# Kernel tuning notes

Measured on AMD Instinct MI355X. Metric: run time of the kernel, lower is better.

## Reference

```python
import jax, jax.numpy as jnp
import numpy as np

B, P, ENC = 64, 196, 512
E, H, A, V, L = 1024, 1024, 512, 20000, 25


def setup_inputs() -> dict:
    key = jax.random.key(0)
    ks = jax.random.split(key, 20)
    s = 0.02
    return {
        "encoder_out": jax.random.normal(ks[0], (B, P, ENC), jnp.float32),
        "captions": jax.random.randint(ks[1], (B, L), 0, V),
        "lengths": L,
        # attention MLP
        "W_enc_att": jax.random.normal(ks[2], (ENC, A), jnp.float32) * s,
        "b_enc_att": jnp.zeros((A,), jnp.float32),
        "W_dec_att": jax.random.normal(ks[3], (H, A), jnp.float32) * s,
        "b_dec_att": jnp.zeros((A,), jnp.float32),
        "W_full_att": jax.random.normal(ks[4], (A, 1), jnp.float32) * s,
        "b_full_att": jnp.zeros((1,), jnp.float32),
        # embedding
        "emb_table": jax.random.normal(ks[5], (V, E), jnp.float32) * s,
        # LSTMCell: input = embedding + context -> (E+ENC, 4H)
        "W_ih": jax.random.normal(ks[6], (E + ENC, 4 * H), jnp.float32) * s,
        "b_ih": jnp.zeros((4 * H,), jnp.float32),
        "W_hh": jax.random.normal(ks[7], (H, 4 * H), jnp.float32) * s,
        "b_hh": jnp.zeros((4 * H,), jnp.float32),
        # init states
        "W_init_h": jax.random.normal(ks[8], (ENC, H), jnp.float32) * s,
        "b_init_h": jnp.zeros((H,), jnp.float32),
        "W_init_c": jax.random.normal(ks[9], (ENC, H), jnp.float32) * s,
        "b_init_c": jnp.zeros((H,), jnp.float32),
        # gate + output proj
        "W_fbeta": jax.random.normal(ks[10], (H, ENC), jnp.float32) * s,
        "b_fbeta": jnp.zeros((ENC,), jnp.float32),
        "W_fc": jax.random.normal(ks[11], (H, V), jnp.float32) * s,
        "b_fc": jnp.zeros((V,), jnp.float32),
    }


def _decode(encoder_out, W_enc_att, b_enc_att, W_dec_att, b_dec_att,
            W_full_att, b_full_att, emb_table, W_ih, b_ih, W_hh, b_hh,
            W_init_h, b_init_h, W_init_c, b_init_c, W_fbeta, b_fbeta,
            W_fc, b_fc, captions, T):
    # precompute encoder-side attention projection (constant across timesteps)
    att_enc = encoder_out @ W_enc_att + b_enc_att          # (B, P, A)
    mean_feat = encoder_out.mean(axis=1)                   # (B, ENC)
    h0 = mean_feat @ W_init_h + b_init_h
    c0 = mean_feat @ W_init_c + b_init_c
    embeddings = emb_table[captions[:, :T]]                # (B, T, E)
    xs = jnp.swapaxes(embeddings, 0, 1)                    # (T, B, E)

    def step(carry, emb_t):
        h, c = carry
        att_dec = h @ W_dec_att + b_dec_att                # (B, A)
        energy = (jax.nn.relu(att_enc + att_dec[:, None, :]) @ W_full_att
                  + b_full_att)[..., 0]                    # (B, P)
        alpha = jax.nn.softmax(energy, axis=1)
        context = jnp.einsum('bp,bpe->be', alpha, encoder_out)
        gate = jax.nn.sigmoid(h @ W_fbeta + b_fbeta)       # (B, ENC)
        x = jnp.concatenate([emb_t, gate * context], axis=1)
        gates = x @ W_ih + b_ih + h @ W_hh + b_hh          # (B, 4H)
        i, f, g, o = jnp.split(gates, 4, axis=1)           # torch order i,f,g,o
        c = jax.nn.sigmoid(f) * c + jax.nn.sigmoid(i) * jnp.tanh(g)
        h = jax.nn.sigmoid(o) * jnp.tanh(c)
        preds = h @ W_fc + b_fc                            # dropout = identity (eval)
        return (h, c), (preds, alpha)

    _, (preds, alphas) = jax.lax.scan(step, (h0, c0), xs)
    predictions = jnp.swapaxes(preds, 0, 1)                # (B, T, V)
    alphas = jnp.swapaxes(alphas, 0, 1)                    # (B, T, P)
    return predictions, alphas


def reference(encoder_out, captions, lengths, W_enc_att, b_enc_att, W_dec_att,
              b_dec_att, W_full_att, b_full_att, emb_table, W_ih, b_ih, W_hh,
              b_hh, W_init_h, b_init_h, W_init_c, b_init_c, W_fbeta, b_fbeta,
              W_fc, b_fc):
    T = int(lengths) - 1
    return _decode(encoder_out, W_enc_att, b_enc_att, W_dec_att, b_dec_att,
                   W_full_att, b_full_att, emb_table, W_ih, b_ih, W_hh, b_hh,
                   W_init_h, b_init_h, W_init_c, b_init_c, W_fbeta, b_fbeta,
                   W_fc, b_fc, captions, T)
```

## Files before the change

### kernel.cpp

```cpp
#include <hip/hip_runtime.h>
#include <hip/hip_bf16.h>

#define BB 64
#define PP 196
#define ENCD 512
#define ED 1024
#define HD 1024
#define AD 512
#define VD 20000
#define TT 24
#define VPAD 20096
#define NSA 4

typedef __attribute__((ext_vector_type(8))) short short8;
typedef __attribute__((ext_vector_type(4))) short short4v;
typedef __attribute__((ext_vector_type(4))) float f32x4;

__device__ __forceinline__ float sigf(float x) { return 1.f / (1.f + __expf(-x)); }

__device__ __forceinline__ unsigned short f2bf(float f) {
    unsigned u = __builtin_bit_cast(unsigned, f);
    u = (u + 0x7FFFu + ((u >> 16) & 1u)) >> 16;
    return (unsigned short)u;
}
__device__ __forceinline__ void split2(float v, unsigned short& h, unsigned short& l) {
    h = f2bf(v);
    float hf = __builtin_bit_cast(float, ((unsigned)h) << 16);
    l = f2bf(v - hf);
}

__global__ __launch_bounds__(256) void split_w_kernel(
    const float* __restrict__ W, unsigned short* __restrict__ oh,
    unsigned short* __restrict__ ol, int N , int Npad, int coff,
    int Nlaunch, int rowoff, int perm) {
    int n = blockIdx.x * 256 + threadIdx.x;
    if (n >= Nlaunch) return;
    int kc = blockIdx.y;
    int src = perm ? ((n & 3) * 1024 + (n >> 2)) : n;
    short8 vh, vl;
    #pragma unroll
    for (int j = 0; j < 8; ++j) {
        float v = (src < N) ? W[(size_t)(rowoff + kc * 8 + j) * N + src] : 0.f;
        unsigned short h, l; split2(v, h, l);
        vh[j] = (short)h; vl[j] = (short)l;
    }
    size_t o = ((size_t)kc * Npad + coff + n) * 8;
    *(short8*)(oh + o) = vh; *(short8*)(ol + o) = vl;
}

__global__ __launch_bounds__(256) void embed_f32_kernel(
    const int* __restrict__ captions, const float* __restrict__ table,
    float* __restrict__ emb_f) {
    int t = blockIdx.x, b = blockIdx.y;
    int tok = captions[b * 25 + t];
    const float4* src = (const float4*)(table + (size_t)tok * ED);
    float4* dst = (float4*)(emb_f + ((size_t)t * BB + b) * ED);
    dst[threadIdx.x] = src[threadIdx.x];
}

__global__ __launch_bounds__(256) void bias_perm_kernel(
    const float* __restrict__ b_ih, const float* __restrict__ b_hh,
    float* __restrict__ out) {
    int n = blockIdx.x * 256 + threadIdx.x;
    int src = (n & 3) * 1024 + (n >> 2);
    out[n] = b_ih[src] + b_hh[src];
}

__global__ __launch_bounds__(512) void mean_kernel(const float* __restrict__ enc,
                                                   float* __restrict__ mf) {
    int b = blockIdx.x; int e = threadIdx.x;
    const float* base = enc + (size_t)b * PP * ENCD + e;
    float s = 0.f;
    #pragma unroll 4
    for (int p = 0; p < PP; ++p) s += base[(size_t)p * ENCD];
    mf[b * ENCD + e] = s * (1.f / PP);
}

__global__ __launch_bounds__(256) void init_hc_kernel(
    const float* __restrict__ mf,
    const float* __restrict__ Wh, const float* __restrict__ bh,
    const float* __restrict__ Wc, const float* __restrict__ bc,
    unsigned short* __restrict__ hc_h, unsigned short* __restrict__ hc_l,
    float* __restrict__ c0) {
    int b = blockIdx.x;
    int isC = blockIdx.y;
    const float* W    = isC ? Wc : Wh;
    const float* bias = isC ? bc : bh;
    __shared__ float smf[ENCD];
    for (int i = threadIdx.x; i < ENCD; i += 256) smf[i] = mf[b * ENCD + i];
    __syncthreads();
    #pragma unroll
    for (int jj = 0; jj < 4; ++jj) {
        int j = threadIdx.x + jj * 256;
        float acc = bias[j];
        for (int k = 0; k < ENCD; ++k) acc += smf[k] * W[(size_t)k * HD + j];
        if (isC) c0[b * HD + j] = acc;
        else {
            unsigned short h, l; split2(acc, h, l);
            size_t o = ((size_t)(j >> 3) * 64 + b) * 8 + (j & 7);
            hc_h[o] = h; hc_l[o] = l;
        }
    }
}

__global__ __launch_bounds__(256) void mfma_gemm_bigf(
    const float* __restrict__ Ap,
    const unsigned short* __restrict__ Bh, const unsigned short* __restrict__ Bl,
    const float* __restrict__ bias, float* __restrict__ C,
    int N, int Npad, int K, int Mtiles, int Ntiles, int inner_m) {
    __shared__ __align__(16) short lds[32768];
    short* Ahs = lds;
    short* Als = lds + 8192;
    short* Bhs = lds + 16384;
    short* Bls = lds + 24576;
    int tid = threadIdx.x, lane = tid & 63, w = tid >> 6;
    int nwg = Mtiles * Ntiles;
    int orig = blockIdx.x;
    int q = nwg >> 3, r = nwg & 7;
    int xcd = orig & 7;
    int basew = (xcd < r) ? xcd * (q + 1) : r * (q + 1) + (xcd - r) * q;
    int wg = basew + (orig >> 3);
    int mt, nt;
    if (inner_m) { mt = wg % Mtiles; nt = wg / Mtiles; }
    else         { nt = wg % Ntiles; mt = wg / Ntiles; }
    int m0 = mt * 128, n0 = nt * 128;
    int wr = w >> 1, wc = w & 1;
    f32x4 acc[4][4];
    #pragma unroll
    for (int i = 0; i < 4; ++i)
        #pragma unroll
        for (int j = 0; j < 4; ++j) acc[i][j] = (f32x4){0.f, 0.f, 0.f, 0.f};
    int nsteps = K >> 6;
    float4 va[8];
    short8 rb[2][4];
    auto load_step = [&](int s) {
        int k0 = s * 64, kc0 = s * 8;
        #pragma unroll
        for (int it = 0; it < 8; ++it) {
            int idx = it * 256 + tid; int m = idx >> 4, k4 = idx & 15;
            va[it] = *(const float4*)(Ap + (size_t)(m0 + m) * K + k0 + k4 * 4);
        }
        #pragma unroll
        for (int it = 0; it < 4; ++it) {
            int g = w * 4 + it; int kcl = g >> 1; int rb0 = (g & 1) * 64;
            size_t gb = ((size_t)(kc0 + kcl) * Npad + n0 + rb0 + lane) * 8;
            rb[0][it] = *(const short8*)(Bh + gb);
            rb[1][it] = *(const short8*)(Bl + gb);
        }
    };
    load_step(0);
    for (int s = 0; s < nsteps; ++s) {
        __syncthreads();
        #pragma unroll
        for (int it = 0; it < 8; ++it) {
            int idx = it * 256 + tid; int m = idx >> 4, k4 = idx & 15;
            int kc = k4 >> 1, jh = (k4 & 1) * 4;
            float vv[4] = {va[it].x, va[it].y, va[it].z, va[it].w};
            short4v hv, lv;
            #pragma unroll
            for (int qq = 0; qq < 4; ++qq) {
                unsigned short h, l; split2(vv[qq], h, l);
                hv[qq] = (short)h; lv[qq] = (short)l;
            }
            int o = kc * 1024 + ((m ^ kc) << 3) + jh;
            *(short4v*)(Ahs + o) = hv;
            *(short4v*)(Als + o) = lv;
        }
        #pragma unroll
        for (int it = 0; it < 4; ++it) {
            int g = w * 4 + it; int kcl = g >> 1; int rb0 = (g & 1) * 64;
            int o = (kcl * 128 + rb0 + lane) * 8;
            *(short8*)(Bhs + o) = rb[0][it];
            *(short8*)(Bls + o) = rb[1][it];
        }
        __syncthreads();
        if (s + 1 < nsteps) load_step(s + 1);
        #pragma unroll
        for (int ks = 0; ks < 2; ++ks) {
            int kq = ks * 4 + (lane >> 4);
            short8 afh[4], afl[4], bfh[4], bfl[4];
            #pragma unroll
            for (int mi = 0; mi < 4; ++mi) {
                int row = wr * 64 + mi * 16 + (lane & 15);
                int o = kq * 1024 + ((row ^ kq) << 3);
                afh[mi] = *(const short8*)(Ahs + o);
                afl[mi] = *(const short8*)(Als + o);
            }
            #pragma unroll
            for (int ni = 0; ni < 4; ++ni) {
                int o = (kq * 128 + wc * 64 + ni * 16 + (lane & 15)) * 8;
                bfh[ni] = *(const short8*)(Bhs + o);
                bfl[ni] = *(const short8*)(Bls + o);
            }
            #pragma unroll
            for (int mi = 0; mi < 4; ++mi)
                #pragma unroll
                for (int ni = 0; ni < 4; ++ni) {
                    acc[mi][ni] = __builtin_amdgcn_mfma_f32_16x16x32_bf16(afh[mi], bfh[ni], acc[mi][ni], 0, 0, 0);
                    acc[mi][ni] = __builtin_amdgcn_mfma_f32_16x16x32_bf16(afh[mi], bfl[ni], acc[mi][ni], 0, 0, 0);
                    acc[mi][ni] = __builtin_amdgcn_mfma_f32_16x16x32_bf16(afl[mi], bfh[ni], acc[mi][ni], 0, 0, 0);
                }
        }
    }
    #pragma unroll
    for (int mi = 0; mi < 4; ++mi) {
        int rrow = m0 + wr * 64 + mi * 16 + ((lane >> 4) << 2);
        #pragma unroll
        for (int ni = 0; ni < 4; ++ni) {
            int c = n0 + wc * 64 + ni * 16 + (lane & 15);
            if (c < N) {
                float bv = bias ? bias[c] : 0.f;
                #pragma unroll
                for (int qq = 0; qq < 4; ++qq)
                    C[(size_t)(rrow + qq) * N + c] = acc[mi][ni][qq] + bv;
            }
        }
    }
}

__global__ __launch_bounds__(256) void mfma_gemm_small(
    const unsigned short* __restrict__ A0h, const unsigned short* __restrict__ A0l,
    const unsigned short* __restrict__ B0h, const unsigned short* __restrict__ B0l,
    float* __restrict__ out, int Npad, int steps) {
    __shared__ __align__(16) short lds[24576];
    short* Ahs = lds;
    short* Als = lds + 4096;
    short* Bhs = lds + 8192;
    short* Bls = lds + 16384;
    int tid = threadIdx.x, lane = tid & 63, w = tid >> 6;
    int n0 = blockIdx.x * 128;
    int kc_base = blockIdx.y * steps * 8;
    out += (size_t)blockIdx.y * 64 * Npad;
    f32x4 acc[4][2];
    #pragma unroll
    for (int i = 0; i < 4; ++i)
        #pragma unroll
        for (int j = 0; j < 2; ++j) acc[i][j] = (f32x4){0.f, 0.f, 0.f, 0.f};
    short8 raa[2][2], rbb[2][4];
    auto load_step = [&](int s) {
        int kc0 = kc_base + s * 8;
        #pragma unroll
        for (int it = 0; it < 2; ++it) {
            int kcl = w * 2 + it; size_t off = ((size_t)(kc0 + kcl) * 64 + lane) * 8;
            raa[0][it] = *(const short8*)(A0h + off);
            raa[1][it] = *(const short8*)(A0l + off);
        }
        #pragma unroll
        for (int it = 0; it < 4; ++it) {
            int g = w * 4 + it; int kcl = g >> 1; int cb = (g & 1) * 64;
            size_t off = ((size_t)(kc0 + kcl) * Npad + n0 + cb + lane) * 8;
            rbb[0][it] = *(const short8*)(B0h + off);
            rbb[1][it] = *(const short8*)(B0l + off);
        }
    };
    load_step(0);
    for (int s = 0; s < steps; ++s) {
        __syncthreads();
        #pragma unroll
        for (int it = 0; it < 2; ++it) {
            int kcl = w * 2 + it; int o = (kcl * 64 + lane) * 8;
            *(short8*)(Ahs + o) = raa[0][it];
            *(short8*)(Als + o) = raa[1][it];
        }
        #pragma unroll
        for (int it = 0; it < 4; ++it) {
            int g = w * 4 + it; int kcl = g >> 1; int cb = (g & 1) * 64;
            int o = (kcl * 128 + cb + lane) * 8;
            *(short8*)(Bhs + o) = rbb[0][it];
            *(short8*)(Bls + o) = rbb[1][it];
        }
        __syncthreads();
        if (s + 1 < steps) load_step(s + 1);
        #pragma unroll
        for (int ks = 0; ks < 2; ++ks) {
            int kq = ks * 4 + (lane >> 4);
            short8 afh[4], afl[4], bfh[2], bfl[2];
            #pragma unroll
            for (int mi = 0; mi < 4; ++mi) {
                int o = (kq * 64 + mi * 16 + (lane & 15)) * 8;
                afh[mi] = *(const short8*)(Ahs + o);
                afl[mi] = *(const short8*)(Als + o);
            }
            #pragma unroll
            for (int ni = 0; ni < 2; ++ni) {
                int o = (kq * 128 + w * 32 + ni * 16 + (lane & 15)) * 8;
                bfh[ni] = *(const short8*)(Bhs + o);
                bfl[ni] = *(const short8*)(Bls + o);
            }
            #pragma unroll
            for (int mi = 0; mi < 4; ++mi)
                #pragma unroll
                for (int ni = 0; ni < 2; ++ni) {
                    acc[mi][ni] = __builtin_amdgcn_mfma_f32_16x16x32_bf16(afh[mi], bfh[ni], acc[mi][ni], 0, 0, 0);
                    acc[mi][ni] = __builtin_amdgcn_mfma_f32_16x16x32_bf16(afh[mi], bfl[ni], acc[mi][ni], 0, 0, 0);
                    acc[mi][ni] = __builtin_amdgcn_mfma_f32_16x16x32_bf16(afl[mi], bfh[ni], acc[mi][ni], 0, 0, 0);
                }
        }
    }
    #pragma unroll
    for (int mi = 0; mi < 4; ++mi) {
        int rrow = mi * 16 + ((lane >> 4) << 2);
        #pragma unroll
        for (int ni = 0; ni < 2; ++ni) {
            int c = n0 + w * 32 + ni * 16 + (lane & 15);
            #pragma unroll
            for (int qq = 0; qq < 4; ++qq)
                out[(size_t)(rrow + qq) * Npad + c] = acc[mi][ni][qq];
        }
    }
}

__global__ __launch_bounds__(1024) void energy_softmax_kernel(
    const float* __restrict__ att_enc, const float* __restrict__ adg,
    const float* __restrict__ b_dec, const float* __restrict__ Wfull,
    float* __restrict__ alpha_out, int t) {
    int b = blockIdx.x; int tid = threadIdx.x;
    __shared__ float sdec[AD], sw[AD], sE[256], red[256];
    if (tid < AD) {
        float s = b_dec[tid];
        #pragma unroll
        for (int ks = 0; ks < NSA; ++ks) s += adg[((size_t)ks * BB + b) * 5120 + tid];
        sdec[tid] = s;
        sw[tid] = Wfull[tid];
    }
    __syncthreads();
    int w = tid >> 6, lane = tid & 63;
    float4 sd0 = *(const float4*)&sdec[lane * 8];
    float4 sd1 = *(const float4*)&sdec[lane * 8 + 4];
    float4 sw0 = *(const float4*)&sw[lane * 8];
    float4 sw1 = *(const float4*)&sw[lane * 8 + 4];
    for (int p = w; p < PP; p += 16) {
        const float* row = att_enc + ((size_t)b * PP + p) * AD + lane * 8;
        float4 v0 = *(const float4*)row;
        float4 v1 = *(const float4*)(row + 4);
        float part = fmaxf(v0.x + sd0.x, 0.f) * sw0.x + fmaxf(v0.y + sd0.y, 0.f) * sw0.y +
                     fmaxf(v0.z + sd0.z, 0.f) * sw0.z + fmaxf(v0.w + sd0.w, 0.f) * sw0.w +
                     fmaxf(v1.x + sd1.x, 0.f) * sw1.x + fmaxf(v1.y + sd1.y, 0.f) * sw1.y +
                     fmaxf(v1.z + sd1.z, 0.f) * sw1.z + fmaxf(v1.w + sd1.w, 0.f) * sw1.w;
        #pragma unroll
        for (int off = 32; off > 0; off >>= 1) part += __shfl_down(part, off, 64);
        if (lane == 0) sE[p] = part;
    }
    __syncthreads();
    float myE = (tid < PP) ? sE[tid] : -1e30f;
    if (tid < 256) red[tid] = myE;
    __syncthreads();
    for (int s = 128; s > 0; s >>= 1) {
        if (tid < s) red[tid] = fmaxf(red[tid], red[tid + s]);
        __syncthreads();
    }
    float mx = red[0];
    __syncthreads();
    float ex = (tid < PP) ? __expf(myE - mx) : 0.f;
    if (tid < 256) red[tid] = ex;
    __syncthreads();
    for (int s = 128; s > 0; s >>= 1) {
        if (tid < s) red[tid] += red[tid + s];
        __syncthreads();
    }
    if (tid < PP) alpha_out[((size_t)b * TT + t) * PP + tid] = ex * (1.f / red[0]);
}

__global__ __launch_bounds__(128) void context_gate_kernel(
    const float* __restrict__ enc, const float* __restrict__ alpha,
    const float* __restrict__ adg, const float* __restrict__ b_fbeta,
    unsigned short* __restrict__ x2h, unsigned short* __restrict__ x2l, int t) {
    int b = blockIdx.x;
    int e = blockIdx.y * 128 + threadIdx.x;
    __shared__ float sal[PP];
    for (int i = threadIdx.x; i < PP; i += 128)
        sal[i] = alpha[((size_t)b * TT + t) * PP + i];
    __syncthreads();
    const float* basep = enc + (size_t)b * PP * ENCD + e;
    float s = 0.f;
    #pragma unroll 4
    for (int p = 0; p < PP; ++p) s += sal[p] * basep[(size_t)p * ENCD];
    float gpre = b_fbeta[e];
    #pragma unroll
    for (int ks = 0; ks < NSA; ++ks) gpre += adg[((size_t)ks * BB + b) * 5120 + 512 + e];
    float gate = sigf(gpre);
    unsigned short h, l; split2(gate * s, h, l);
    size_t o = ((size_t)(e >> 3) * 64 + b) * 8 + (e & 7);
    x2h[o] = h; x2l[o] = l;
}

__global__ __launch_bounds__(128) void gates_lstm_kernel(
    const unsigned short* __restrict__ Ah, const unsigned short* __restrict__ Al,
    const unsigned short* __restrict__ Bh, const unsigned short* __restrict__ Bl,
    const float* __restrict__ pregates, const float* __restrict__ adg,
    float* __restrict__ c, unsigned short* __restrict__ hc_h,
    unsigned short* __restrict__ hc_l, float* __restrict__ h_all, int t) {
    __shared__ __align__(16) short lds[12288];
    __shared__ float gl[64][36];
    short* Ahs = lds;
    short* Als = lds + 4096;
    short* Bhs = lds + 8192;
    short* Bls = lds + 10240;
    int tid = threadIdx.x, lane = tid & 63, w = tid >> 6;
    int n0 = blockIdx.x * 32;
    f32x4 acc[4];
    #pragma unroll
    for (int i = 0; i < 4; ++i) acc[i] = (f32x4){0.f, 0.f, 0.f, 0.f};
    short8 ra[2][4], rb[2][2];
    auto load_step = [&](int s) {
        int kc0 = s * 8;
        #pragma unroll
        for (int it = 0; it < 4; ++it) {
            int idx = it * 128 + tid; int kcl = idx >> 6, row = idx & 63;
            size_t off = ((size_t)(kc0 + kcl) * 64 + row) * 8;
            ra[0][it] = *(const short8*)(Ah + off);
            ra[1][it] = *(const short8*)(Al + off);
        }
        #pragma unroll
        for (int it = 0; it < 2; ++it) {
            int idx = it * 128 + tid; int kcl = idx >> 5, col = idx & 31;
            size_t off = ((size_t)(kc0 + kcl) * 4096 + n0 + col) * 8;
            rb[0][it] = *(const short8*)(Bh + off);
            rb[1][it] = *(const short8*)(Bl + off);
        }
    };
    load_step(0);
    for (int s = 0; s < 8; ++s) {
        __syncthreads();
        #pragma unroll
        for (int it = 0; it < 4; ++it) {
            int idx = it * 128 + tid; int kcl = idx >> 6, row = idx & 63;
            int o = (kcl * 64 + row) * 8;
            *(short8*)(Ahs + o) = ra[0][it];
            *(short8*)(Als + o) = ra[1][it];
        }
        #pragma unroll
        for (int it = 0; it < 2; ++it) {
            int idx = it * 128 + tid; int kcl = idx >> 5, col = idx & 31;
            int o = (kcl * 32 + col) * 8;
            *(short8*)(Bhs + o) = rb[0][it];
            *(short8*)(Bls + o) = rb[1][it];
        }
        __syncthreads();
        if (s + 1 < 8) load_step(s + 1);
        #pragma unroll
        for (int ks = 0; ks < 2; ++ks) {
            int kq = ks * 4 + (lane >> 4);
            short8 afh[4], afl[4], bfh, bfl;
            #pragma unroll
            for (int mi = 0; mi < 4; ++mi) {
                int o = (kq * 64 + mi * 16 + (lane & 15)) * 8;
                afh[mi] = *(const short8*)(Ahs + o);
                afl[mi] = *(const short8*)(Als + o);
            }
            int ob = (kq * 32 + w * 16 + (lane & 15)) * 8;
            bfh = *(const short8*)(Bhs + ob);
            bfl = *(const short8*)(Bls + ob);
            #pragma unroll
            for (int mi = 0; mi < 4; ++mi) {
                acc[mi] = __builtin_amdgcn_mfma_f32_16x16x32_bf16(afh[mi], bfh, acc[mi], 0, 0, 0);
                acc[mi] = __builtin_amdgcn_mfma_f32_16x16x32_bf16(afh[mi], bfl, acc[mi], 0, 0, 0);
                acc[mi] = __builtin_amdgcn_mfma_f32_16x16x32_bf16(afl[mi], bfh, acc[mi], 0, 0, 0);
            }
        }
    }
    int cL = w * 16 + (lane & 15);
    #pragma unroll
    for (int mi = 0; mi < 4; ++mi) {
        #pragma unroll
        for (int qq = 0; qq < 4; ++qq) {
            int b = mi * 16 + ((lane >> 4) << 2) + qq;
            float val = acc[mi][qq] + pregates[((size_t)(t * 64 + b)) * 4096 + n0 + cL];
            #pragma unroll
            for (int ks = 0; ks < NSA; ++ks)
                val += adg[((size_t)ks * BB + b) * 5120 + 1024 + n0 + cL];
            gl[b][cL] = val;
        }
    }
    __syncthreads();
    #pragma unroll
    for (int i = 0; i < 4; ++i) {
        int idx = tid + i * 128;
        int b = idx >> 3, jl = idx & 7;
        float iG = gl[b][4 * jl + 0], fG = gl[b][4 * jl + 1];
        float gG = gl[b][4 * jl + 2], oG = gl[b][4 * jl + 3];
        int j = (n0 >> 2) + jl;
        float cn = sigf(fG) * c[b * HD + j] + sigf(iG) * tanhf(gG);
        c[b * HD + j] = cn;
        float hn = sigf(oG) * tanhf(cn);
        unsigned short h, l; split2(hn, h, l);
        size_t o1 = ((size_t)(j >> 3) * 64 + b) * 8 + (j & 7);
        hc_h[o1] = h; hc_l[o1] = l;
        h_all[((size_t)b * TT + t) * HD + j] = hn;
    }
}

extern "C" void kernel_launch(void* const* d_in, const int* in_sizes, int n_in,
                              void* d_out, int out_size, void* d_ws, size_t ws_size,
                              hipStream_t stream) {
    const float* enc      = (const float*)d_in[0];
    const int*   captions = (const int*)d_in[1];
    const float* W_enc    = (const float*)d_in[3];
    const float* b_enc    = (const float*)d_in[4];
    const float* W_dec    = (const float*)d_in[5];
    const float* b_dec    = (const float*)d_in[6];
    const float* W_full   = (const float*)d_in[7];
    const float* table    = (const float*)d_in[9];
    const float* W_ih     = (const float*)d_in[10];
    const float* b_ih     = (const float*)d_in[11];
    const float* W_hh     = (const float*)d_in[12];
    const float* b_hh     = (const float*)d_in[13];
    const float* W_init_h = (const float*)d_in[14];
    const float* b_init_h = (const float*)d_in[15];
    const float* W_init_c = (const float*)d_in[16];
    const float* b_init_c = (const float*)d_in[17];
    const float* W_fbeta  = (const float*)d_in[18];
    const float* b_fbeta  = (const float*)d_in[19];
    const float* W_fc     = (const float*)d_in[20];
    const float* b_fc     = (const float*)d_in[21];

    float* preds  = (float*)d_out;
    float* alphas = (float*)d_out + (size_t)BB * TT * VD;

    char* base = (char*)d_ws;
    size_t off = 0;
    auto take = [&](size_t b) { void* r = (void*)(base + off); off += (b + 255) & ~(size_t)255; return r; };
    float* att_enc = (float*)take((size_t)12544 * 512 * 4);
    unsigned short* wbig_h = (unsigned short*)take((size_t)128 * 5120 * 8 * 2);
    unsigned short* wbig_l = (unsigned short*)take((size_t)128 * 5120 * 8 * 2);
    unsigned short* wih2_h = (unsigned short*)take((size_t)64 * 4096 * 8 * 2);
    unsigned short* wih2_l = (unsigned short*)take((size_t)64 * 4096 * 8 * 2);
    float* pregates = (float*)take((size_t)TT * BB * 4096 * 4);
    float* adg      = (float*)take((size_t)NSA * BB * 5120 * 4);
    unsigned short* wfc_h = (unsigned short*)(base);
    unsigned short* wfc_l = (unsigned short*)(base + (size_t)128 * VPAD * 8 * 2);
    unsigned short* wih1_h = (unsigned short*)take((size_t)128 * 4096 * 8 * 2);
    unsigned short* wih1_l = (unsigned short*)take((size_t)128 * 4096 * 8 * 2);
    unsigned short* wenc_h = (unsigned short*)take((size_t)64 * 512 * 8 * 2);
    unsigned short* wenc_l = (unsigned short*)take((size_t)64 * 512 * 8 * 2);
    float* emb_f    = (float*)take((size_t)TT * BB * ED * 4);
    float* biasp    = (float*)take((size_t)4096 * 4);
    float* c_buf = (float*)take((size_t)BB * HD * 4);
    float* mf    = (float*)take((size_t)BB * ENCD * 4);
    unsigned short* x2c_h = (unsigned short*)take((size_t)64 * 64 * 8 * 2);
    unsigned short* x2c_l = (unsigned short*)take((size_t)64 * 64 * 8 * 2);
    unsigned short* hc_h  = (unsigned short*)take((size_t)128 * 64 * 8 * 2);
    unsigned short* hc_l  = (unsigned short*)take((size_t)128 * 64 * 8 * 2);
    float* h_all = (float*)take((size_t)TT * BB * HD * 4);

    split_w_kernel<<<dim3(2, 64), 256, 0, stream>>>(W_enc, wenc_h, wenc_l, 512, 512, 0, 512, 0, 0);
    split_w_kernel<<<dim3(2, 128), 256, 0, stream>>>(W_dec, wbig_h, wbig_l, 512, 5120, 0, 512, 0, 0);
    split_w_kernel<<<dim3(2, 128), 256, 0, stream>>>(W_fbeta, wbig_h, wbig_l, 512, 5120, 512, 512, 0, 0);
    split_w_kernel<<<dim3(16, 128), 256, 0, stream>>>(W_hh, wbig_h, wbig_l, 4096, 5120, 1024, 4096, 0, 1);
    split_w_kernel<<<dim3(16, 128), 256, 0, stream>>>(W_ih, wih1_h, wih1_l, 4096, 4096, 0, 4096, 0, 1);
    split_w_kernel<<<dim3(16, 64), 256, 0, stream>>>(W_ih, wih2_h, wih2_l, 4096, 4096, 0, 4096, 1024, 1);
    bias_perm_kernel<<<16, 256, 0, stream>>>(b_ih, b_hh, biasp);
    embed_f32_kernel<<<dim3(TT, BB), 256, 0, stream>>>(captions, table, emb_f);
    mean_kernel<<<BB, 512, 0, stream>>>(enc, mf);
    init_hc_kernel<<<dim3(BB, 2), 256, 0, stream>>>(mf, W_init_h, b_init_h, W_init_c, b_init_c,
                                                    hc_h, hc_l, c_buf);
    mfma_gemm_bigf<<<392, 256, 0, stream>>>(enc, wenc_h, wenc_l, b_enc, att_enc,
                                            512, 512, 512, 98, 4, 0);
    mfma_gemm_bigf<<<384, 256, 0, stream>>>(emb_f, wih1_h, wih1_l, biasp, pregates,
                                            4096, 4096, 1024, 12, 32, 1);

    for (int t = 0; t < TT; ++t) {
        mfma_gemm_small<<<dim3(40, NSA), 256, 0, stream>>>(hc_h, hc_l, wbig_h, wbig_l,
                                                           adg, 5120, 4);
        energy_softmax_kernel<<<BB, 1024, 0, stream>>>(att_enc, adg, b_dec, W_full, alphas, t);
        context_gate_kernel<<<dim3(BB, 4), 128, 0, stream>>>(enc, alphas, adg, b_fbeta,
                                                             x2c_h, x2c_l, t);
        gates_lstm_kernel<<<128, 128, 0, stream>>>(x2c_h, x2c_l, wih2_h, wih2_l,
                                                   pregates, adg, c_buf, hc_h, hc_l, h_all, t);
    }

    split_w_kernel<<<dim3(79, 128), 256, 0, stream>>>(W_fc, wfc_h, wfc_l, VD, VPAD, 0, VPAD, 0, 0);
    mfma_gemm_bigf<<<1884, 256, 0, stream>>>(h_all, wfc_h, wfc_l, b_fc, preds,
                                             VD, VPAD, 1024, 12, 157, 1);
}
```

Before: 1.565 ms.

## Fuse context into attention kernel and move W_hh into LSTM gates GEMM

Energy/softmax and context-gate kernels are merged into one per-batch kernel, dropping a launch per timestep and the alpha round trip through global memory. The W_hh recurrent product moves out of the shared small GEMM and into the gates kernel by concatenating the context and previous h into one K=1536 operand with ping-pong buffers. The small GEMM now computes only the 1024 attention/gate columns. The gates kernel uses narrower N tiles across 256 blocks and splits K between its two waves, reducing per-step sync work at the cost of a longer serial K loop per block.

```diff
diff --git a/kernel.cpp b/kernel.cpp
--- a/kernel.cpp
+++ b/kernel.cpp
@@ -10,7 +10,7 @@
 #define VD 20000
 #define TT 24
 #define VPAD 20096
-#define NSA 4
+#define HOFF 32768
 
 typedef __attribute__((ext_vector_type(8))) short short8;
 typedef __attribute__((ext_vector_type(4))) short short4v;
@@ -310,18 +310,27 @@
     }
 }
 
-__global__ __launch_bounds__(1024) void energy_softmax_kernel(
+__global__ __launch_bounds__(1024) void attn_ctx_kernel(
     const float* __restrict__ att_enc, const float* __restrict__ adg,
     const float* __restrict__ b_dec, const float* __restrict__ Wfull,
-    float* __restrict__ alpha_out, int t) {
+    const float* __restrict__ enc, const float* __restrict__ b_fbeta,
+    float* __restrict__ alpha_out, unsigned short* __restrict__ x2h,
+    unsigned short* __restrict__ x2l, int t) {
     int b = blockIdx.x; int tid = threadIdx.x;
-    __shared__ float sdec[AD], sw[AD], sE[256], red[256];
+    __shared__ float sdec[AD], sw[AD], sgate[AD], sal[256], sE[256], red[256];
+    __shared__ float sctx[2][AD];
     if (tid < AD) {
         float s = b_dec[tid];
         #pragma unroll
-        for (int ks = 0; ks < NSA; ++ks) s += adg[((size_t)ks * BB + b) * 5120 + tid];
+        for (int ks = 0; ks < 8; ++ks) s += adg[((size_t)ks * BB + b) * 1024 + tid];
         sdec[tid] = s;
         sw[tid] = Wfull[tid];
+    } else {
+        int e = tid - AD;
+        float s = b_fbeta[e];
+        #pragma unroll
+        for (int ks = 0; ks < 8; ++ks) s += adg[((size_t)ks * BB + b) * 1024 + AD + e];
+        sgate[e] = s;
     }
     __syncthreads();
     int w = tid >> 6, lane = tid & 63;
@@ -358,50 +367,46 @@
         if (tid < s) red[tid] += red[tid + s];
         __syncthreads();
     }
-    if (tid < PP) alpha_out[((size_t)b * TT + t) * PP + tid] = ex * (1.f / red[0]);
-}
-
-__global__ __launch_bounds__(128) void context_gate_kernel(
-    const float* __restrict__ enc, const float* __restrict__ alpha,
-    const float* __restrict__ adg, const float* __restrict__ b_fbeta,
-    unsigned short* __restrict__ x2h, unsigned short* __restrict__ x2l, int t) {
-    int b = blockIdx.x;
-    int e = blockIdx.y * 128 + threadIdx.x;
-    __shared__ float sal[PP];
-    for (int i = threadIdx.x; i < PP; i += 128)
-        sal[i] = alpha[((size_t)b * TT + t) * PP + i];
-    __syncthreads();
+    if (tid < PP) {
+        float al = ex * (1.f / red[0]);
+        sal[tid] = al;
+        alpha_out[((size_t)b * TT + t) * PP + tid] = al;
+    }
+    __syncthreads();
+    int e = tid & 511, half = tid >> 9;
     const float* basep = enc + (size_t)b * PP * ENCD + e;
-    float s = 0.f;
-    #pragma unroll 4
-    for (int p = 0; p < PP; ++p) s += sal[p] * basep[(size_t)p * ENCD];
-    float gpre = b_fbeta[e];
-    #pragma unroll
-    for (int ks = 0; ks < NSA; ++ks) gpre += adg[((size_t)ks * BB + b) * 5120 + 512 + e];
-    float gate = sigf(gpre);
-    unsigned short h, l; split2(gate * s, h, l);
-    size_t o = ((size_t)(e >> 3) * 64 + b) * 8 + (e & 7);
-    x2h[o] = h; x2l[o] = l;
+    float s2 = 0.f;
+    #pragma unroll 2
+    for (int p = half * 98; p < half * 98 + 98; ++p) s2 += sal[p] * basep[(size_t)p * ENCD];
+    sctx[half][e] = s2;
+    __syncthreads();
+    if (tid < AD) {
+        float ctx = sctx[0][tid] + sctx[1][tid];
+        float gate = sigf(sgate[tid]);
+        unsigned short h, l; split2(gate * ctx, h, l);
+        size_t o = ((size_t)(tid >> 3) * 64 + b) * 8 + (tid & 7);
+        x2h[o] = h; x2l[o] = l;
+    }
 }
 
 __global__ __launch_bounds__(128) void gates_lstm_kernel(
     const unsigned short* __restrict__ Ah, const unsigned short* __restrict__ Al,
     const unsigned short* __restrict__ Bh, const unsigned short* __restrict__ Bl,
-    const float* __restrict__ pregates, const float* __restrict__ adg,
-    float* __restrict__ c, unsigned short* __restrict__ hc_h,
-    unsigned short* __restrict__ hc_l, float* __restrict__ h_all, int t) {
-    __shared__ __align__(16) short lds[12288];
-    __shared__ float gl[64][36];
+    const float* __restrict__ pregates, float* __restrict__ c,
+    unsigned short* __restrict__ ho_h, unsigned short* __restrict__ ho_l,
+    float* __restrict__ h_all, int t) {
+    __shared__ __align__(16) short lds[10240];
+    __shared__ float gl[64][17];
     short* Ahs = lds;
     short* Als = lds + 4096;
     short* Bhs = lds + 8192;
-    short* Bls = lds + 10240;
+    short* Bls = lds + 9216;
     int tid = threadIdx.x, lane = tid & 63, w = tid >> 6;
-    int n0 = blockIdx.x * 32;
+    int n0 = blockIdx.x * 16;
     f32x4 acc[4];
     #pragma unroll
     for (int i = 0; i < 4; ++i) acc[i] = (f32x4){0.f, 0.f, 0.f, 0.f};
-    short8 ra[2][4], rb[2][2];
+    short8 ra[2][4], rb[2];
     auto load_step = [&](int s) {
         int kc0 = s * 8;
         #pragma unroll
@@ -411,16 +416,15 @@
             ra[0][it] = *(const short8*)(Ah + off);
             ra[1][it] = *(const short8*)(Al + off);
         }
-        #pragma unroll
-        for (int it = 0; it < 2; ++it) {
-            int idx = it * 128 + tid; int kcl = idx >> 5, col = idx & 31;
+        {
+            int kcl = tid >> 4, col = tid & 15;
             size_t off = ((size_t)(kc0 + kcl) * 4096 + n0 + col) * 8;
-            rb[0][it] = *(const short8*)(Bh + off);
-            rb[1][it] = *(const short8*)(Bl + off);
+            rb[0] = *(const short8*)(Bh + off);
+            rb[1] = *(const short8*)(Bl + off);
         }
     };
     load_step(0);
-    for (int s = 0; s < 8; ++s) {
+    for (int s = 0; s < 24; ++s) {
         __syncthreads();
         #pragma unroll
         for (int it = 0; it < 4; ++it) {
@@ -429,64 +433,64 @@
             *(short8*)(Ahs + o) = ra[0][it];
             *(short8*)(Als + o) = ra[1][it];
         }
-        #pragma unroll
-        for (int it = 0; it < 2; ++it) {
-            int idx = it * 128 + tid; int kcl = idx >> 5, col = idx & 31;
-            int o = (kcl * 32 + col) * 8;
-            *(short8*)(Bhs + o) = rb[0][it];
-            *(short8*)(Bls + o) = rb[1][it];
-        }
-        __syncthreads();
-        if (s + 1 < 8) load_step(s + 1);
-        #pragma unroll
-        for (int ks = 0; ks < 2; ++ks) {
-            int kq = ks * 4 + (lane >> 4);
-            short8 afh[4], afl[4], bfh, bfl;
-            #pragma unroll
-            for (int mi = 0; mi < 4; ++mi) {
-                int o = (kq * 64 + mi * 16 + (lane & 15)) * 8;
-                afh[mi] = *(const short8*)(Ahs + o);
-                afl[mi] = *(const short8*)(Als + o);
-            }
-            int ob = (kq * 32 + w * 16 + (lane & 15)) * 8;
-            bfh = *(const short8*)(Bhs + ob);
-            bfl = *(const short8*)(Bls + ob);
-            #pragma unroll
-            for (int mi = 0; mi < 4; ++mi) {
-                acc[mi] = __builtin_amdgcn_mfma_f32_16x16x32_bf16(afh[mi], bfh, acc[mi], 0, 0, 0);
-                acc[mi] = __builtin_amdgcn_mfma_f32_16x16x32_bf16(afh[mi], bfl, acc[mi], 0, 0, 0);
-                acc[mi] = __builtin_amdgcn_mfma_f32_16x16x32_bf16(afl[mi], bfh, acc[mi], 0, 0, 0);
-            }
-        }
-    }
-    int cL = w * 16 + (lane & 15);
-    #pragma unroll
-    for (int mi = 0; mi < 4; ++mi) {
-        #pragma unroll
-        for (int qq = 0; qq < 4; ++qq) {
-            int b = mi * 16 + ((lane >> 4) << 2) + qq;
-            float val = acc[mi][qq] + pregates[((size_t)(t * 64 + b)) * 4096 + n0 + cL];
-            #pragma unroll
-            for (int ks = 0; ks < NSA; ++ks)
-                val += adg[((size_t)ks * BB + b) * 5120 + 1024 + n0 + cL];
-            gl[b][cL] = val;
-        }
-    }
-    __syncthreads();
-    #pragma unroll
-    for (int i = 0; i < 4; ++i) {
+        {
+            int kcl = tid >> 4, col = tid & 15;
+            int o = (kcl * 16 + col) * 8;
+            *(short8*)(Bhs + o) = rb[0];
+            *(short8*)(Bls + o) = rb[1];
+        }
+        __syncthreads();
+        if (s + 1 < 24) load_step(s + 1);
+        int kq = w * 4 + (lane >> 4);
+        short8 afh[4], afl[4], bfh, bfl;
+        #pragma unroll
+        for (int mi = 0; mi < 4; ++mi) {
+            int o = (kq * 64 + mi * 16 + (lane & 15)) * 8;
+            afh[mi] = *(const short8*)(Ahs + o);
+            afl[mi] = *(const short8*)(Als + o);
+        }
+        int ob = (kq * 16 + (lane & 15)) * 8;
+        bfh = *(const short8*)(Bhs + ob);
+        bfl = *(const short8*)(Bls + ob);
+        #pragma unroll
+        for (int mi = 0; mi < 4; ++mi) {
+            acc[mi] = __builtin_amdgcn_mfma_f32_16x16x32_bf16(afh[mi], bfh, acc[mi], 0, 0, 0);
+            acc[mi] = __builtin_amdgcn_mfma_f32_16x16x32_bf16(afh[mi], bfl, acc[mi], 0, 0, 0);
+            acc[mi] = __builtin_amdgcn_mfma_f32_16x16x32_bf16(afl[mi], bfh, acc[mi], 0, 0, 0);
+        }
+    }
+    if (w == 0) {
+        #pragma unroll
+        for (int mi = 0; mi < 4; ++mi)
+            #pragma unroll
+            for (int qq = 0; qq < 4; ++qq)
+                gl[mi * 16 + ((lane >> 4) << 2) + qq][lane & 15] = acc[mi][qq];
+    }
+    __syncthreads();
+    if (w == 1) {
+        #pragma unroll
+        for (int mi = 0; mi < 4; ++mi)
+            #pragma unroll
+            for (int qq = 0; qq < 4; ++qq) {
+                int r = mi * 16 + ((lane >> 4) << 2) + qq, cl = lane & 15;
+                gl[r][cl] += acc[mi][qq] + pregates[((size_t)(t * 64 + r)) * 4096 + n0 + cl];
+            }
+    }
+    __syncthreads();
+    #pragma unroll
+    for (int i = 0; i < 2; ++i) {
         int idx = tid + i * 128;
-        int b = idx >> 3, jl = idx & 7;
-        float iG = gl[b][4 * jl + 0], fG = gl[b][4 * jl + 1];
-        float gG = gl[b][4 * jl + 2], oG = gl[b][4 * jl + 3];
+        int bb = idx >> 2, jl = idx & 3;
+        float iG = gl[bb][4 * jl + 0], fG = gl[bb][4 * jl + 1];
+        float gG = gl[bb][4 * jl + 2], oG = gl[bb][4 * jl + 3];
         int j = (n0 >> 2) + jl;
-        float cn = sigf(fG) * c[b * HD + j] + sigf(iG) * tanhf(gG);
-        c[b * HD + j] = cn;
+        float cn = sigf(fG) * c[bb * HD + j] + sigf(iG) * tanhf(gG);
+        c[bb * HD + j] = cn;
         float hn = sigf(oG) * tanhf(cn);
         unsigned short h, l; split2(hn, h, l);
-        size_t o1 = ((size_t)(j >> 3) * 64 + b) * 8 + (j & 7);
-        hc_h[o1] = h; hc_l[o1] = l;
-        h_all[((size_t)b * TT + t) * HD + j] = hn;
+        size_t o1 = ((size_t)(j >> 3) * 64 + bb) * 8 + (j & 7);
+        ho_h[o1] = h; ho_l[o1] = l;
+        h_all[((size_t)bb * TT + t) * HD + j] = hn;
     }
 }
 
@@ -521,52 +525,56 @@
     size_t off = 0;
     auto take = [&](size_t b) { void* r = (void*)(base + off); off += (b + 255) & ~(size_t)255; return r; };
     float* att_enc = (float*)take((size_t)12544 * 512 * 4);
-    unsigned short* wbig_h = (unsigned short*)take((size_t)128 * 5120 * 8 * 2);
-    unsigned short* wbig_l = (unsigned short*)take((size_t)128 * 5120 * 8 * 2);
-    unsigned short* wih2_h = (unsigned short*)take((size_t)64 * 4096 * 8 * 2);
-    unsigned short* wih2_l = (unsigned short*)take((size_t)64 * 4096 * 8 * 2);
+    unsigned short* wih1_h = (unsigned short*)take((size_t)128 * 4096 * 8 * 2);
+    unsigned short* wih1_l = (unsigned short*)take((size_t)128 * 4096 * 8 * 2);
+    unsigned short* wg2_h  = (unsigned short*)take((size_t)192 * 4096 * 8 * 2);
+    unsigned short* wg2_l  = (unsigned short*)take((size_t)192 * 4096 * 8 * 2);
+    unsigned short* watt_h = (unsigned short*)take((size_t)128 * 1024 * 8 * 2);
+    unsigned short* watt_l = (unsigned short*)take((size_t)128 * 1024 * 8 * 2);
+    unsigned short* wenc_h = (unsigned short*)take((size_t)64 * 512 * 8 * 2);
+    unsigned short* wenc_l = (unsigned short*)take((size_t)64 * 512 * 8 * 2);
     float* pregates = (float*)take((size_t)TT * BB * 4096 * 4);
-    float* adg      = (float*)take((size_t)NSA * BB * 5120 * 4);
+    float* adg      = (float*)take((size_t)8 * BB * 1024 * 4);
+    float* emb_f    = (float*)take((size_t)TT * BB * ED * 4);
+    float* biasp    = (float*)take((size_t)4096 * 4);
     unsigned short* wfc_h = (unsigned short*)(base);
     unsigned short* wfc_l = (unsigned short*)(base + (size_t)128 * VPAD * 8 * 2);
-    unsigned short* wih1_h = (unsigned short*)take((size_t)128 * 4096 * 8 * 2);
-    unsigned short* wih1_l = (unsigned short*)take((size_t)128 * 4096 * 8 * 2);
-    unsigned short* wenc_h = (unsigned short*)take((size_t)64 * 512 * 8 * 2);
-    unsigned short* wenc_l = (unsigned short*)take((size_t)64 * 512 * 8 * 2);
-    float* emb_f    = (float*)take((size_t)TT * BB * ED * 4);
-    float* biasp    = (float*)take((size_t)4096 * 4);
     float* c_buf = (float*)take((size_t)BB * HD * 4);
     float* mf    = (float*)take((size_t)BB * ENCD * 4);
-    unsigned short* x2c_h = (unsigned short*)take((size_t)64 * 64 * 8 * 2);
-    unsigned short* x2c_l = (unsigned short*)take((size_t)64 * 64 * 8 * 2);
-    unsigned short* hc_h  = (unsigned short*)take((size_t)128 * 64 * 8 * 2);
-    unsigned short* hc_l  = (unsigned short*)take((size_t)128 * 64 * 8 * 2);
+    unsigned short* axh_h[2], *axh_l[2];
+    axh_h[0] = (unsigned short*)take((size_t)192 * 64 * 8 * 2);
+    axh_l[0] = (unsigned short*)take((size_t)192 * 64 * 8 * 2);
+    axh_h[1] = (unsigned short*)take((size_t)192 * 64 * 8 * 2);
+    axh_l[1] = (unsigned short*)take((size_t)192 * 64 * 8 * 2);
     float* h_all = (float*)take((size_t)TT * BB * HD * 4);
 
     split_w_kernel<<<dim3(2, 64), 256, 0, stream>>>(W_enc, wenc_h, wenc_l, 512, 512, 0, 512, 0, 0);
-    split_w_kernel<<<dim3(2, 128), 256, 0, stream>>>(W_dec, wbig_h, wbig_l, 512, 5120, 0, 512, 0, 0);
-    split_w_kernel<<<dim3(2, 128), 256, 0, stream>>>(W_fbeta, wbig_h, wbig_l, 512, 5120, 512, 512, 0, 0);
-    split_w_kernel<<<dim3(16, 128), 256, 0, stream>>>(W_hh, wbig_h, wbig_l, 4096, 5120, 1024, 4096, 0, 1);
+    split_w_kernel<<<dim3(2, 128), 256, 0, stream>>>(W_dec, watt_h, watt_l, 512, 1024, 0, 512, 0, 0);
+    split_w_kernel<<<dim3(2, 128), 256, 0, stream>>>(W_fbeta, watt_h, watt_l, 512, 1024, 512, 512, 0, 0);
     split_w_kernel<<<dim3(16, 128), 256, 0, stream>>>(W_ih, wih1_h, wih1_l, 4096, 4096, 0, 4096, 0, 1);
-    split_w_kernel<<<dim3(16, 64), 256, 0, stream>>>(W_ih, wih2_h, wih2_l, 4096, 4096, 0, 4096, 1024, 1);
+    split_w_kernel<<<dim3(16, 64), 256, 0, stream>>>(W_ih, wg2_h, wg2_l, 4096, 4096, 0, 4096, 1024, 1);
+    split_w_kernel<<<dim3(16, 128), 256, 0, stream>>>(W_hh, wg2_h + (size_t)64 * 4096 * 8,
+                                                      wg2_l + (size_t)64 * 4096 * 8,
+                                                      4096, 4096, 0, 4096, 0, 1);
     bias_perm_kernel<<<16, 256, 0, stream>>>(b_ih, b_hh, biasp);
     embed_f32_kernel<<<dim3(TT, BB), 256, 0, stream>>>(captions, table, emb_f);
     mean_kernel<<<BB, 512, 0, stream>>>(enc, mf);
     init_hc_kernel<<<dim3(BB, 2), 256, 0, stream>>>(mf, W_init_h, b_init_h, W_init_c, b_init_c,
-                                                    hc_h, hc_l, c_buf);
+                                                    axh_h[0] + HOFF, axh_l[0] + HOFF, c_buf);
     mfma_gemm_bigf<<<392, 256, 0, stream>>>(enc, wenc_h, wenc_l, b_enc, att_enc,
                                             512, 512, 512, 98, 4, 0);
     mfma_gemm_bigf<<<384, 256, 0, stream>>>(emb_f, wih1_h, wih1_l, biasp, pregates,
                                             4096, 4096, 1024, 12, 32, 1);
 
     for (int t = 0; t < TT; ++t) {
-        mfma_gemm_small<<<dim3(40, NSA), 256, 0, stream>>>(hc_h, hc_l, wbig_h, wbig_l,
-                                                           adg, 5120, 4);
-        energy_softmax_kernel<<<BB, 1024, 0, stream>>>(att_enc, adg, b_dec, W_full, alphas, t);
-        context_gate_kernel<<<dim3(BB, 4), 128, 0, stream>>>(enc, alphas, adg, b_fbeta,
-                                                             x2c_h, x2c_l, t);
-        gates_lstm_kernel<<<128, 128, 0, stream>>>(x2c_h, x2c_l, wih2_h, wih2_l,
-                                                   pregates, adg, c_buf, hc_h, hc_l, h_all, t);
+        int par = t & 1;
+        mfma_gemm_small<<<dim3(8, 8), 256, 0, stream>>>(
+            axh_h[par] + HOFF, axh_l[par] + HOFF, watt_h, watt_l, adg, 1024, 2);
+        attn_ctx_kernel<<<BB, 1024, 0, stream>>>(att_enc, adg, b_dec, W_full, enc, b_fbeta,
+                                                 alphas, axh_h[par], axh_l[par], t);
+        gates_lstm_kernel<<<256, 128, 0, stream>>>(
+            axh_h[par], axh_l[par], wg2_h, wg2_l, pregates, c_buf,
+            axh_h[1 - par] + HOFF, axh_l[1 - par] + HOFF, h_all, t);
     }
 
     split_w_kernel<<<dim3(79, 128), 256, 0, stream>>>(W_fc, wfc_h, wfc_l, VD, VPAD, 0, VPAD, 0, 0);
```

Result: slower. 1.622 ms (+3.7%).
